# Kernel tuning notes

Measured on AMD Instinct MI355X. Metric: run time of the kernel, lower is better.

The kernel has to match this reference:

```python
import jax, jax.numpy as jnp
import numpy as np

D_MODEL = 256
N_LEVELS = 4
N_HEADS = 8
N_POINTS = 4
D_HEAD = D_MODEL // N_HEADS  # 32
BATCH = 8
SHAPES = np.array([[64, 64], [32, 32], [16, 16], [8, 8]], dtype=np.int32)
LEN_IN = int((SHAPES[:, 0] * SHAPES[:, 1]).sum())  # 5440
LEN_Q = LEN_IN
STARTS = np.concatenate([[0], np.cumsum(SHAPES[:, 0] * SHAPES[:, 1])[:-1]]).astype(np.int32)


def _offset_bias():
    # faithful _reset_parameters grid init for sampling_offsets bias
    thetas = np.arange(N_HEADS, dtype=np.float64) * (2.0 * np.pi / N_HEADS)
    grid = np.stack([np.cos(thetas), np.sin(thetas)], -1)
    grid = grid / np.abs(grid).max(-1, keepdims=True)
    grid = np.tile(grid[:, None, None, :], (1, N_LEVELS, N_POINTS, 1))
    grid = grid * (np.arange(N_POINTS) + 1)[None, None, :, None]
    return jnp.asarray(grid.reshape(-1), dtype=jnp.float32)


def setup_inputs() -> dict:
    key = jax.random.key(0)
    ks = jax.random.split(key, 8)
    s = 1.0 / np.sqrt(D_MODEL)
    return {
        "query": jax.random.normal(ks[0], (BATCH, LEN_Q, D_MODEL), jnp.float32),
        "reference_points": jax.random.uniform(ks[1], (BATCH, LEN_Q, N_LEVELS, 2), jnp.float32),
        "input_flatten": jax.random.normal(ks[2], (BATCH, LEN_IN, D_MODEL), jnp.float32),
        "input_spatial_shapes": jnp.asarray(SHAPES),
        "input_level_start_index": jnp.asarray(STARTS),
        "W_val": jax.random.normal(ks[3], (D_MODEL, D_MODEL), jnp.float32) * s,
        "b_val": jnp.zeros((D_MODEL,), jnp.float32),
        "W_off": jax.random.normal(ks[4], (D_MODEL, N_HEADS * N_LEVELS * N_POINTS * 2), jnp.float32) * 0.01,
        "b_off": _offset_bias(),
        "W_attn": jax.random.normal(ks[5], (D_MODEL, N_HEADS * N_LEVELS * N_POINTS), jnp.float32) * s,
        "b_attn": jnp.zeros((N_HEADS * N_LEVELS * N_POINTS,), jnp.float32),
        "W_out": jax.random.normal(ks[6], (D_MODEL, D_MODEL), jnp.float32) * s,
        "b_out": jnp.zeros((D_MODEL,), jnp.float32),
    }


def _ms_deform_attn_core(value, shapes_np, starts_np, sampling_locations, attention_weights):
    # value: (N, Lin, Hn, d); sampling_locations: (N, Lq, Hn, L, P, 2) in [0,1]
    # attention_weights: (N, Lq, Hn, L, P)
    n, lq = sampling_locations.shape[:2]
    value_t = jnp.transpose(value, (0, 2, 1, 3))  # (N, Hn, Lin, d)
    out = jnp.zeros((n, N_HEADS, lq, value.shape[-1]), value.dtype)
    for lvl in range(N_LEVELS):
        H, W = int(shapes_np[lvl, 0]), int(shapes_np[lvl, 1])
        st = int(starts_np[lvl])
        v = value_t[:, :, st:st + H * W]  # (N, Hn, H*W, d)
        loc = jnp.transpose(sampling_locations[:, :, :, lvl], (0, 2, 1, 3, 4))  # (N, Hn, Lq, P, 2)
        x = loc[..., 0] * W - 0.5
        y = loc[..., 1] * H - 0.5
        x0 = jnp.floor(x).astype(jnp.int32)
        y0 = jnp.floor(y).astype(jnp.int32)
        lx = x - x0
        ly = y - y0
        x1, y1 = x0 + 1, y0 + 1

        def gather(yc, xc):
            valid = (yc >= 0) & (yc < H) & (xc >= 0) & (xc < W)
            idx = jnp.clip(yc, 0, H - 1) * W + jnp.clip(xc, 0, W - 1)
            idx = idx.reshape(n, N_HEADS, -1)  # (N, Hn, Lq*P)
            g = jnp.take_along_axis(v, idx[..., None], axis=2)  # (N, Hn, Lq*P, d)
            return g * valid.reshape(n, N_HEADS, -1, 1)

        w00 = ((1 - lx) * (1 - ly)).reshape(n, N_HEADS, -1, 1)
        w01 = (lx * (1 - ly)).reshape(n, N_HEADS, -1, 1)
        w10 = ((1 - lx) * ly).reshape(n, N_HEADS, -1, 1)
        w11 = (lx * ly).reshape(n, N_HEADS, -1, 1)
        samp = (gather(y0, x0) * w00 + gather(y0, x1) * w01 +
                gather(y1, x0) * w10 + gather(y1, x1) * w11)
        samp = samp.reshape(n, N_HEADS, lq, N_POINTS, -1)
        aw = jnp.transpose(attention_weights[:, :, :, lvl], (0, 2, 1, 3))  # (N, Hn, Lq, P)
        out = out + (samp * aw[..., None]).sum(axis=3)
    return jnp.transpose(out, (0, 2, 1, 3)).reshape(n, lq, -1)


def reference(query, reference_points, input_flatten, input_spatial_shapes,
              input_level_start_index, W_val, b_val, W_off, b_off,
              W_attn, b_attn, W_out, b_out):
    shapes_np = np.asarray(input_spatial_shapes)
    starts_np = np.asarray(input_level_start_index)
    n, lq, _ = query.shape
    lin = input_flatten.shape[1]

    value = (input_flatten @ W_val + b_val).reshape(n, lin, N_HEADS, D_HEAD)
    off = (query @ W_off + b_off).reshape(n, lq, N_HEADS, N_LEVELS, N_POINTS, 2)
    attn = jax.nn.softmax((query @ W_attn + b_attn).reshape(n, lq, N_HEADS, N_LEVELS * N_POINTS), axis=-1)
    attn = attn.reshape(n, lq, N_HEADS, N_LEVELS, N_POINTS)

    # normalizer: (L, 2) as [W, H]
    normalizer = jnp.stack([input_spatial_shapes[:, 1], input_spatial_shapes[:, 0]], -1).astype(query.dtype)
    loc = reference_points[:, :, None, :, None, :] + off / normalizer[None, None, None, :, None, :]

    out = _ms_deform_attn_core(value, shapes_np, starts_np, loc, attn)
    return out @ W_out + b_out
```

## Files before the change

kernel.cpp:

```cpp
#include <hip/hip_runtime.h>

typedef unsigned short ushort;
typedef unsigned int uint;
typedef __bf16 bf16x8 __attribute__((ext_vector_type(8)));
typedef float floatx4 __attribute__((ext_vector_type(4)));
typedef ushort ushort8 __attribute__((ext_vector_type(8)));

constexpr int LQ = 5440;
constexpr int ROWS = 43520;

__device__ __forceinline__ ushort f2b(float f) {
  union { float f; uint i; } v; v.f = f;
  uint r = v.i + 0x7FFFu + ((v.i >> 16) & 1u);
  return (ushort)(r >> 16);
}
__device__ __forceinline__ float blo(uint u) {
  union { uint i; float f; } v; v.i = u << 16; return v.f;
}
__device__ __forceinline__ float bhi(uint u) {
  union { uint i; float f; } v; v.i = u & 0xFFFF0000u; return v.f;
}

__global__ __launch_bounds__(256) void wcast_kernel(
    const float* __restrict__ Wv, const float* __restrict__ Wo,
    const float* __restrict__ Wa, const float* __restrict__ Wu,
    ushort* __restrict__ Wt) {
  int k = threadIdx.x;
  int n = blockIdx.x;
  int m = blockIdx.y;
  const float* src = (m == 0) ? Wv : (m == 1) ? Wo : (m == 2) ? Wa : Wu;
  int N = (m == 2) ? 128 : 256;
  if (n >= N) return;
  size_t off = (size_t)m * 65536 - ((m == 3) ? 32768 : 0);
  Wt[off + (size_t)n * 256 + k] = f2b(src[(size_t)k * N + n]);
}

template<bool ABF16>
__device__ __forceinline__ void mfma_128x128(
    const void* __restrict__ Av, const ushort* __restrict__ Bt,
    int row_base, int n0, ushort* At, ushort* Bs, floatx4 (&acc)[4][4]) {
  const int t = threadIdx.x;
  const int r = t >> 1, half = t & 1;
  const int lane = t & 63, wv = t >> 6;
  const int quad = lane >> 4, l15 = lane & 15;
  const int m0w = (wv >> 1) * 64, n0w = (wv & 1) * 64;
#pragma unroll
  for (int i = 0; i < 4; ++i)
#pragma unroll
    for (int j = 0; j < 4; ++j) acc[i][j] = floatx4{0.f, 0.f, 0.f, 0.f};

  for (int k0 = 0; k0 < 256; k0 += 32) {
    if (ABF16) {
      const ushort* ap = (const ushort*)Av + (size_t)(row_base + r) * 256 + k0 + half * 16;
      *(ushort8*)&At[r * 32 + half * 16]     = *(const ushort8*)ap;
      *(ushort8*)&At[r * 32 + half * 16 + 8] = *(const ushort8*)(ap + 8);
    } else {
      const float* ap = (const float*)Av + (size_t)(row_base + r) * 256 + k0 + half * 16;
      float4 a0 = *(const float4*)ap,       a1 = *(const float4*)(ap + 4);
      float4 a2 = *(const float4*)(ap + 8), a3 = *(const float4*)(ap + 12);
      ushort8 u0, u1;
      u0[0] = f2b(a0.x); u0[1] = f2b(a0.y); u0[2] = f2b(a0.z); u0[3] = f2b(a0.w);
      u0[4] = f2b(a1.x); u0[5] = f2b(a1.y); u0[6] = f2b(a1.z); u0[7] = f2b(a1.w);
      u1[0] = f2b(a2.x); u1[1] = f2b(a2.y); u1[2] = f2b(a2.z); u1[3] = f2b(a2.w);
      u1[4] = f2b(a3.x); u1[5] = f2b(a3.y); u1[6] = f2b(a3.z); u1[7] = f2b(a3.w);
      *(ushort8*)&At[r * 32 + half * 16]     = u0;
      *(ushort8*)&At[r * 32 + half * 16 + 8] = u1;
    }
    {
      const ushort* bp = Bt + (size_t)(n0 + r) * 256 + k0 + half * 16;
      *(ushort8*)&Bs[r * 32 + half * 16]     = *(const ushort8*)bp;
      *(ushort8*)&Bs[r * 32 + half * 16 + 8] = *(const ushort8*)(bp + 8);
    }
    __syncthreads();
    bf16x8 af[4], bfv[4];
#pragma unroll
    for (int ti = 0; ti < 4; ++ti)
      af[ti] = *(const bf16x8*)&At[(m0w + ti * 16 + l15) * 32 + quad * 8];
#pragma unroll
    for (int tj = 0; tj < 4; ++tj)
      bfv[tj] = *(const bf16x8*)&Bs[(n0w + tj * 16 + l15) * 32 + quad * 8];
#pragma unroll
    for (int ti = 0; ti < 4; ++ti)
#pragma unroll
      for (int tj = 0; tj < 4; ++tj)
        acc[ti][tj] = __builtin_amdgcn_mfma_f32_16x16x32_bf16(af[ti], bfv[tj], acc[ti][tj], 0, 0, 0);
    __syncthreads();
  }
}

__global__ __launch_bounds__(256) void gemm_val_kernel(
    const float* __restrict__ X, const ushort* __restrict__ WtV,
    const float* __restrict__ bval, ushort* __restrict__ value) {
  __shared__ ushort At[4096];
  __shared__ ushort Bs[4096];
  floatx4 acc[4][4];
  int row_base = blockIdx.x * 128, n0 = blockIdx.y * 128;
  mfma_128x128<false>(X, WtV, row_base, n0, At, Bs, acc);
  const int t = threadIdx.x, lane = t & 63, wv = t >> 6;
  const int quad = lane >> 4, l15 = lane & 15;
  const int m0w = (wv >> 1) * 64, n0w = (wv & 1) * 64;
#pragma unroll
  for (int tj = 0; tj < 4; ++tj) {
    int gcol = n0 + n0w + tj * 16 + l15;
    float b = bval[gcol];
#pragma unroll
    for (int ti = 0; ti < 4; ++ti)
#pragma unroll
      for (int reg = 0; reg < 4; ++reg) {
        int grow = row_base + m0w + ti * 16 + quad * 4 + reg;
        value[(size_t)grow * 256 + gcol] = f2b(acc[ti][tj][reg] + b);
      }
  }
}

__global__ __launch_bounds__(256) void gemm_off_kernel(
    const float* __restrict__ Q, const ushort* __restrict__ WtO,
    const float* __restrict__ boff, const float* __restrict__ refp,
    float* __restrict__ tblf) {
  __shared__ ushort At[4096];
  __shared__ ushort Bs[4096];
  floatx4 acc[4][4];
  int row_base = blockIdx.x * 128, n0 = blockIdx.y * 128;
  mfma_128x128<false>(Q, WtO, row_base, n0, At, Bs, acc);
  const int t = threadIdx.x, lane = t & 63, wv = t >> 6;
  const int quad = lane >> 4, l15 = lane & 15;
  const int m0w = (wv >> 1) * 64, n0w = (wv & 1) * 64;
#pragma unroll
  for (int tj = 0; tj < 4; ++tj) {
    int gcol = n0 + n0w + tj * 16 + l15;
    float b = boff[gcol];
    int pair = gcol >> 1, xy = gcol & 1;
    int hh = pair >> 4, lp = pair & 15, l = lp >> 2;
    float lw = (float)(64 >> l);
#pragma unroll
    for (int ti = 0; ti < 4; ++ti)
#pragma unroll
      for (int reg = 0; reg < 4; ++reg) {
        int grow = row_base + m0w + ti * 16 + quad * 4 + reg;
        float ref = refp[(size_t)grow * 8 + l * 2 + xy];
        float o = acc[ti][tj][reg] + b;
        tblf[(((size_t)grow * 8 + hh) * 16 + lp) * 4 + xy] = ref * lw + o - 0.5f;
      }
  }
}

__global__ __launch_bounds__(256) void gemm_attn_kernel(
    const float* __restrict__ Q, const ushort* __restrict__ WtA,
    const float* __restrict__ battn, uint4* __restrict__ tbl) {
  __shared__ ushort At[4096];
  __shared__ ushort Bs[4096];
  floatx4 acc[4][4];
  int row_base = blockIdx.x * 128;
  mfma_128x128<false>(Q, WtA, row_base, 0, At, Bs, acc);
  const int t = threadIdx.x, lane = t & 63, wv = t >> 6;
  const int quad = lane >> 4, l15 = lane & 15;
  const int m0w = (wv >> 1) * 64;
  const int headbase = (wv & 1) * 4;
  const int lp = l15, l = lp >> 2;
  const int wd = 64 >> l;
  const int st = (l >= 1 ? 4096 : 0) + (l >= 2 ? 1024 : 0) + (l >= 3 ? 256 : 0);
#pragma unroll
  for (int tj = 0; tj < 4; ++tj) {
    int h = headbase + tj;
    float bia = battn[h * 16 + lp];
#pragma unroll
    for (int ti = 0; ti < 4; ++ti)
#pragma unroll
      for (int reg = 0; reg < 4; ++reg) {
        int grow = row_base + m0w + ti * 16 + quad * 4 + reg;
        float x = acc[ti][tj][reg] + bia;
        float m = x;
        m = fmaxf(m, __shfl_xor(m, 1, 64));
        m = fmaxf(m, __shfl_xor(m, 2, 64));
        m = fmaxf(m, __shfl_xor(m, 4, 64));
        m = fmaxf(m, __shfl_xor(m, 8, 64));
        float e = __expf(x - m);
        float s = e;
        s += __shfl_xor(s, 1, 64);
        s += __shfl_xor(s, 2, 64);
        s += __shfl_xor(s, 4, 64);
        s += __shfl_xor(s, 8, 64);
        float aw = e / s;
        uint4* slot = &tbl[((size_t)grow * 8 + h) * 16 + lp];
        uint4 sv = *slot;
        float xx = __uint_as_float(sv.x), yy = __uint_as_float(sv.y);
        float fx = floorf(xx), fy = floorf(yy);
        float lx = xx - fx, ly = yy - fy;
        int x0 = (int)fx, y0 = (int)fy, x1 = x0 + 1, y1 = y0 + 1;
        int cx0 = min(max(x0, 0), wd - 1), cx1 = min(max(x1, 0), wd - 1);
        int cy0 = min(max(y0, 0), wd - 1), cy1 = min(max(y1, 0), wd - 1);
        float vx0 = (x0 >= 0 && x0 < wd) ? 1.f : 0.f;
        float vx1 = (x1 >= 0 && x1 < wd) ? 1.f : 0.f;
        float vy0 = (y0 >= 0 && y0 < wd) ? 1.f : 0.f;
        float vy1 = (y1 >= 0 && y1 < wd) ? 1.f : 0.f;
        float g00 = (1.f - lx) * (1.f - ly) * vx0 * vy0 * aw;
        float g01 = lx * (1.f - ly) * vx1 * vy0 * aw;
        float g10 = (1.f - lx) * ly * vx0 * vy1 * aw;
        float g11 = lx * ly * vx1 * vy1 * aw;
        uint i00 = st + cy0 * wd + cx0, i01 = st + cy0 * wd + cx1;
        uint i10 = st + cy1 * wd + cx0, i11 = st + cy1 * wd + cx1;
        uint4 ov;
        ov.x = i00 | (i01 << 16);
        ov.y = i10 | (i11 << 16);
        ov.z = (uint)f2b(g00) | ((uint)f2b(g01) << 16);
        ov.w = (uint)f2b(g10) | ((uint)f2b(g11) << 16);
        *slot = ov;
      }
  }
}

__global__ __launch_bounds__(512) void core_kernel(
    const ushort* __restrict__ value, const uint* __restrict__ tbl,
    uint* __restrict__ coreo) {
  const int brow = blockIdx.x;
  const int b = brow / LQ;
  const int t = threadIdx.x;
  const int h = t >> 6, lane = t & 63;
  const int d2 = lane & 15;
  const uint v = tbl[((size_t)brow * 8 + h) * 64 + lane];
  const uint* vb = (const uint*)(value + (size_t)b * (LQ * 256)) + h * 16 + d2;
  float acc0 = 0.f, acc1 = 0.f;
#pragma unroll
  for (int j = 0; j < 4; ++j) {
    uint i01 = (uint)__shfl((int)v, (lane & 48) | (4 * j + 0), 64);
    uint i23 = (uint)__shfl((int)v, (lane & 48) | (4 * j + 1), 64);
    uint wab = (uint)__shfl((int)v, (lane & 48) | (4 * j + 2), 64);
    uint wcd = (uint)__shfl((int)v, (lane & 48) | (4 * j + 3), 64);
    uint s00 = vb[(i01 & 0xFFFFu) * 128];
    uint s01 = vb[(i01 >> 16) * 128];
    uint s10 = vb[(i23 & 0xFFFFu) * 128];
    uint s11 = vb[(i23 >> 16) * 128];
    float f00 = blo(wab), f01 = bhi(wab), f10 = blo(wcd), f11 = bhi(wcd);
    acc0 = fmaf(f00, blo(s00), acc0); acc1 = fmaf(f00, bhi(s00), acc1);
    acc0 = fmaf(f01, blo(s01), acc0); acc1 = fmaf(f01, bhi(s01), acc1);
    acc0 = fmaf(f10, blo(s10), acc0); acc1 = fmaf(f10, bhi(s10), acc1);
    acc0 = fmaf(f11, blo(s11), acc0); acc1 = fmaf(f11, bhi(s11), acc1);
  }
  acc0 += __shfl_xor(acc0, 16, 64); acc0 += __shfl_xor(acc0, 32, 64);
  acc1 += __shfl_xor(acc1, 16, 64); acc1 += __shfl_xor(acc1, 32, 64);
  if (lane < 16) {
    uint p = (uint)f2b(acc0) | ((uint)f2b(acc1) << 16);
    coreo[((size_t)brow * 8 + h) * 16 + d2] = p;
  }
}

__global__ __launch_bounds__(256) void gemm_out_kernel(
    const ushort* __restrict__ C, const ushort* __restrict__ WtU,
    const float* __restrict__ bout, float* __restrict__ out) {
  __shared__ ushort At[4096];
  __shared__ ushort Bs[4096];
  floatx4 acc[4][4];
  int row_base = blockIdx.x * 128, n0 = blockIdx.y * 128;
  mfma_128x128<true>(C, WtU, row_base, n0, At, Bs, acc);
  const int t = threadIdx.x, lane = t & 63, wv = t >> 6;
  const int quad = lane >> 4, l15 = lane & 15;
  const int m0w = (wv >> 1) * 64, n0w = (wv & 1) * 64;
#pragma unroll
  for (int tj = 0; tj < 4; ++tj) {
    int gcol = n0 + n0w + tj * 16 + l15;
    float b = bout[gcol];
#pragma unroll
    for (int ti = 0; ti < 4; ++ti)
#pragma unroll
      for (int reg = 0; reg < 4; ++reg) {
        int grow = row_base + m0w + ti * 16 + quad * 4 + reg;
        out[(size_t)grow * 256 + gcol] = acc[ti][tj][reg] + b;
      }
  }
}

extern "C" void kernel_launch(void* const* d_in, const int* in_sizes, int n_in,
                              void* d_out, int out_size, void* d_ws, size_t ws_size,
                              hipStream_t stream) {
  const float* query  = (const float*)d_in[0];
  const float* refp   = (const float*)d_in[1];
  const float* inpf   = (const float*)d_in[2];
  const float* W_val  = (const float*)d_in[5];
  const float* b_val  = (const float*)d_in[6];
  const float* W_off  = (const float*)d_in[7];
  const float* b_off  = (const float*)d_in[8];
  const float* W_attn = (const float*)d_in[9];
  const float* b_attn = (const float*)d_in[10];
  const float* W_out  = (const float*)d_in[11];
  const float* b_out  = (const float*)d_in[12];

  char* ws = (char*)d_ws;
  ushort* Wt    = (ushort*)ws;
  ushort* value = (ushort*)(ws + 1048576);
  uint*   tbl   = (uint*)(ws + 1048576 + 22282240);
  uint*   coreo = (uint*)(ws + 1048576 + 22282240 + 89128960);

  dim3 blk(256);
  wcast_kernel    <<<dim3(256, 4), blk, 0, stream>>>(W_val, W_off, W_attn, W_out, Wt);
  gemm_val_kernel <<<dim3(ROWS / 128, 2), blk, 0, stream>>>(inpf, Wt, b_val, value);
  gemm_off_kernel <<<dim3(ROWS / 128, 2), blk, 0, stream>>>(query, Wt + 65536, b_off, refp, (float*)tbl);
  gemm_attn_kernel<<<dim3(ROWS / 128, 1), blk, 0, stream>>>(query, Wt + 131072, b_attn, (uint4*)tbl);
  core_kernel     <<<dim3(ROWS), dim3(512), 0, stream>>>(value, tbl, coreo);
  gemm_out_kernel <<<dim3(ROWS / 128, 2), blk, 0, stream>>>((const ushort*)coreo, Wt + 163840, b_out, (float*)d_out);
}
```

Measured before the change: 387.8 us.

## Precast activations to bf16, retile attn GEMM, widen core gathers, batch-interleave rows

Adds a precast kernel that converts query and input_flatten to bf16 once, so the GEMMs stop re-converting fp32 tiles inside their K loops (query had been converted twice, by the off and attn GEMMs). The attention GEMM now uses 64-row tiles and stages its logits through shared memory so each thread does a full 16-way softmax without shuffles. The value and offset epilogues pack pairs of outputs into wider stores. The core gather kernel reads 8-byte uint2 chunks, interleaves blocks across batches, and reuses workspace regions. The precast adds an extra pass over the fp32 inputs, and the workspace aliasing depends on kernel ordering being correct.

New measurement: 443.1 us. 1.14x slower.

```diff
diff --git a/kernel.cpp b/kernel.cpp
--- a/kernel.cpp
+++ b/kernel.cpp
@@ -19,6 +19,21 @@
 }
 __device__ __forceinline__ float bhi(uint u) {
   union { uint i; float f; } v; v.i = u & 0xFFFF0000u; return v.f;
+}
+
+__global__ __launch_bounds__(256) void precast_kernel(
+    const float* __restrict__ q, const float* __restrict__ x,
+    ushort* __restrict__ qb, ushort* __restrict__ ib) {
+  int bx = blockIdx.x;
+  const float* src; ushort* dst;
+  if (bx < 5440) { src = q; dst = qb; } else { src = x; dst = ib; bx -= 5440; }
+  size_t i = ((size_t)bx * 256 + threadIdx.x) * 8;
+  float4 a = *(const float4*)(src + i);
+  float4 b = *(const float4*)(src + i + 4);
+  ushort8 o;
+  o[0] = f2b(a.x); o[1] = f2b(a.y); o[2] = f2b(a.z); o[3] = f2b(a.w);
+  o[4] = f2b(b.x); o[5] = f2b(b.y); o[6] = f2b(b.z); o[7] = f2b(b.w);
+  *(ushort8*)(dst + i) = o;
 }
 
 __global__ __launch_bounds__(256) void wcast_kernel(
@@ -35,9 +50,8 @@
   Wt[off + (size_t)n * 256 + k] = f2b(src[(size_t)k * N + n]);
 }
 
-template<bool ABF16>
-__device__ __forceinline__ void mfma_128x128(
-    const void* __restrict__ Av, const ushort* __restrict__ Bt,
+__device__ __forceinline__ void mfma_tile128(
+    const ushort* __restrict__ Ab, const ushort* __restrict__ Bt,
     int row_base, int n0, ushort* At, ushort* Bs, floatx4 (&acc)[4][4]) {
   const int t = threadIdx.x;
   const int r = t >> 1, half = t & 1;
@@ -50,21 +64,10 @@
     for (int j = 0; j < 4; ++j) acc[i][j] = floatx4{0.f, 0.f, 0.f, 0.f};
 
   for (int k0 = 0; k0 < 256; k0 += 32) {
-    if (ABF16) {
-      const ushort* ap = (const ushort*)Av + (size_t)(row_base + r) * 256 + k0 + half * 16;
+    {
+      const ushort* ap = Ab + (size_t)(row_base + r) * 256 + k0 + half * 16;
       *(ushort8*)&At[r * 32 + half * 16]     = *(const ushort8*)ap;
       *(ushort8*)&At[r * 32 + half * 16 + 8] = *(const ushort8*)(ap + 8);
-    } else {
-      const float* ap = (const float*)Av + (size_t)(row_base + r) * 256 + k0 + half * 16;
-      float4 a0 = *(const float4*)ap,       a1 = *(const float4*)(ap + 4);
-      float4 a2 = *(const float4*)(ap + 8), a3 = *(const float4*)(ap + 12);
-      ushort8 u0, u1;
-      u0[0] = f2b(a0.x); u0[1] = f2b(a0.y); u0[2] = f2b(a0.z); u0[3] = f2b(a0.w);
-      u0[4] = f2b(a1.x); u0[5] = f2b(a1.y); u0[6] = f2b(a1.z); u0[7] = f2b(a1.w);
-      u1[0] = f2b(a2.x); u1[1] = f2b(a2.y); u1[2] = f2b(a2.z); u1[3] = f2b(a2.w);
-      u1[4] = f2b(a3.x); u1[5] = f2b(a3.y); u1[6] = f2b(a3.z); u1[7] = f2b(a3.w);
-      *(ushort8*)&At[r * 32 + half * 16]     = u0;
-      *(ushort8*)&At[r * 32 + half * 16 + 8] = u1;
     }
     {
       const ushort* bp = Bt + (size_t)(n0 + r) * 256 + k0 + half * 16;
@@ -89,13 +92,13 @@
 }
 
 __global__ __launch_bounds__(256) void gemm_val_kernel(
-    const float* __restrict__ X, const ushort* __restrict__ WtV,
-    const float* __restrict__ bval, ushort* __restrict__ value) {
+    const ushort* __restrict__ Xb, const ushort* __restrict__ WtV,
+    const float* __restrict__ bval, uint* __restrict__ value32) {
   __shared__ ushort At[4096];
   __shared__ ushort Bs[4096];
   floatx4 acc[4][4];
   int row_base = blockIdx.x * 128, n0 = blockIdx.y * 128;
-  mfma_128x128<false>(X, WtV, row_base, n0, At, Bs, acc);
+  mfma_tile128(Xb, WtV, row_base, n0, At, Bs, acc);
   const int t = threadIdx.x, lane = t & 63, wv = t >> 6;
   const int quad = lane >> 4, l15 = lane & 15;
   const int m0w = (wv >> 1) * 64, n0w = (wv & 1) * 64;
@@ -108,20 +111,25 @@
 #pragma unroll
       for (int reg = 0; reg < 4; ++reg) {
         int grow = row_base + m0w + ti * 16 + quad * 4 + reg;
-        value[(size_t)grow * 256 + gcol] = f2b(acc[ti][tj][reg] + b);
+        float val = acc[ti][tj][reg] + b;
+        float part = __shfl_xor(val, 1, 64);
+        if ((l15 & 1) == 0) {
+          uint p = (uint)f2b(val) | ((uint)f2b(part) << 16);
+          value32[(size_t)grow * 128 + (gcol >> 1)] = p;
+        }
       }
   }
 }
 
 __global__ __launch_bounds__(256) void gemm_off_kernel(
-    const float* __restrict__ Q, const ushort* __restrict__ WtO,
+    const ushort* __restrict__ Qb, const ushort* __restrict__ WtO,
     const float* __restrict__ boff, const float* __restrict__ refp,
     float* __restrict__ tblf) {
   __shared__ ushort At[4096];
   __shared__ ushort Bs[4096];
   floatx4 acc[4][4];
   int row_base = blockIdx.x * 128, n0 = blockIdx.y * 128;
-  mfma_128x128<false>(Q, WtO, row_base, n0, At, Bs, acc);
+  mfma_tile128(Qb, WtO, row_base, n0, At, Bs, acc);
   const int t = threadIdx.x, lane = t & 63, wv = t >> 6;
   const int quad = lane >> 4, l15 = lane & 15;
   const int m0w = (wv >> 1) * 64, n0w = (wv & 1) * 64;
@@ -138,109 +146,162 @@
       for (int reg = 0; reg < 4; ++reg) {
         int grow = row_base + m0w + ti * 16 + quad * 4 + reg;
         float ref = refp[(size_t)grow * 8 + l * 2 + xy];
-        float o = acc[ti][tj][reg] + b;
-        tblf[(((size_t)grow * 8 + hh) * 16 + lp) * 4 + xy] = ref * lw + o - 0.5f;
+        float pos = ref * lw + (acc[ti][tj][reg] + b) - 0.5f;
+        float part = __shfl_xor(pos, 1, 64);
+        if ((l15 & 1) == 0) {
+          float2 o; o.x = pos; o.y = part;
+          *(float2*)(tblf + (((size_t)grow * 8 + hh) * 16 + lp) * 4) = o;
+        }
       }
   }
 }
 
+union KU {
+  struct { ushort At[2048]; ushort Bs[4096]; } g;
+  float ct[64 * 132];
+  __device__ KU() {}
+};
 __global__ __launch_bounds__(256) void gemm_attn_kernel(
-    const float* __restrict__ Q, const ushort* __restrict__ WtA,
-    const float* __restrict__ battn, uint4* __restrict__ tbl) {
-  __shared__ ushort At[4096];
-  __shared__ ushort Bs[4096];
-  floatx4 acc[4][4];
-  int row_base = blockIdx.x * 128;
-  mfma_128x128<false>(Q, WtA, row_base, 0, At, Bs, acc);
-  const int t = threadIdx.x, lane = t & 63, wv = t >> 6;
-  const int quad = lane >> 4, l15 = lane & 15;
-  const int m0w = (wv >> 1) * 64;
-  const int headbase = (wv & 1) * 4;
-  const int lp = l15, l = lp >> 2;
-  const int wd = 64 >> l;
-  const int st = (l >= 1 ? 4096 : 0) + (l >= 2 ? 1024 : 0) + (l >= 3 ? 256 : 0);
-#pragma unroll
-  for (int tj = 0; tj < 4; ++tj) {
-    int h = headbase + tj;
-    float bia = battn[h * 16 + lp];
-#pragma unroll
-    for (int ti = 0; ti < 4; ++ti)
-#pragma unroll
-      for (int reg = 0; reg < 4; ++reg) {
-        int grow = row_base + m0w + ti * 16 + quad * 4 + reg;
-        float x = acc[ti][tj][reg] + bia;
-        float m = x;
-        m = fmaxf(m, __shfl_xor(m, 1, 64));
-        m = fmaxf(m, __shfl_xor(m, 2, 64));
-        m = fmaxf(m, __shfl_xor(m, 4, 64));
-        m = fmaxf(m, __shfl_xor(m, 8, 64));
-        float e = __expf(x - m);
-        float s = e;
-        s += __shfl_xor(s, 1, 64);
-        s += __shfl_xor(s, 2, 64);
-        s += __shfl_xor(s, 4, 64);
-        s += __shfl_xor(s, 8, 64);
-        float aw = e / s;
-        uint4* slot = &tbl[((size_t)grow * 8 + h) * 16 + lp];
-        uint4 sv = *slot;
-        float xx = __uint_as_float(sv.x), yy = __uint_as_float(sv.y);
-        float fx = floorf(xx), fy = floorf(yy);
-        float lx = xx - fx, ly = yy - fy;
-        int x0 = (int)fx, y0 = (int)fy, x1 = x0 + 1, y1 = y0 + 1;
-        int cx0 = min(max(x0, 0), wd - 1), cx1 = min(max(x1, 0), wd - 1);
-        int cy0 = min(max(y0, 0), wd - 1), cy1 = min(max(y1, 0), wd - 1);
-        float vx0 = (x0 >= 0 && x0 < wd) ? 1.f : 0.f;
-        float vx1 = (x1 >= 0 && x1 < wd) ? 1.f : 0.f;
-        float vy0 = (y0 >= 0 && y0 < wd) ? 1.f : 0.f;
-        float vy1 = (y1 >= 0 && y1 < wd) ? 1.f : 0.f;
-        float g00 = (1.f - lx) * (1.f - ly) * vx0 * vy0 * aw;
-        float g01 = lx * (1.f - ly) * vx1 * vy0 * aw;
-        float g10 = (1.f - lx) * ly * vx0 * vy1 * aw;
-        float g11 = lx * ly * vx1 * vy1 * aw;
-        uint i00 = st + cy0 * wd + cx0, i01 = st + cy0 * wd + cx1;
-        uint i10 = st + cy1 * wd + cx0, i11 = st + cy1 * wd + cx1;
-        uint4 ov;
-        ov.x = i00 | (i01 << 16);
-        ov.y = i10 | (i11 << 16);
-        ov.z = (uint)f2b(g00) | ((uint)f2b(g01) << 16);
-        ov.w = (uint)f2b(g10) | ((uint)f2b(g11) << 16);
-        *slot = ov;
-      }
+    const ushort* __restrict__ Qb, const ushort* __restrict__ WtA,
+    const float* __restrict__ battn, uint4* __restrict__ tblq) {
+  __shared__ KU u;
+  floatx4 acc[8];
+  const int t = threadIdx.x;
+  const int lane = t & 63, wv = t >> 6;
+  const int quad = lane >> 4, l15 = lane & 15;
+  int row_base = blockIdx.x * 64;
+#pragma unroll
+  for (int j = 0; j < 8; ++j) acc[j] = floatx4{0.f, 0.f, 0.f, 0.f};
+
+  for (int k0 = 0; k0 < 256; k0 += 32) {
+    {
+      int r = t >> 2, seg = t & 3;
+      *(ushort8*)&u.g.At[r * 32 + seg * 8] =
+          *(const ushort8*)(Qb + (size_t)(row_base + r) * 256 + k0 + seg * 8);
+    }
+#pragma unroll
+    for (int i = 0; i < 2; ++i) {
+      int item = t + 256 * i;
+      int r = item >> 2, seg = item & 3;
+      *(ushort8*)&u.g.Bs[r * 32 + seg * 8] =
+          *(const ushort8*)(WtA + (size_t)r * 256 + k0 + seg * 8);
+    }
+    __syncthreads();
+    bf16x8 af = *(const bf16x8*)&u.g.At[(wv * 16 + l15) * 32 + quad * 8];
+#pragma unroll
+    for (int tj = 0; tj < 8; ++tj) {
+      bf16x8 bf = *(const bf16x8*)&u.g.Bs[(tj * 16 + l15) * 32 + quad * 8];
+      acc[tj] = __builtin_amdgcn_mfma_f32_16x16x32_bf16(af, bf, acc[tj], 0, 0, 0);
+    }
+    __syncthreads();
+  }
+#pragma unroll
+  for (int tj = 0; tj < 8; ++tj) {
+    int col = tj * 16 + l15;
+    float bb = battn[col];
+#pragma unroll
+    for (int reg = 0; reg < 4; ++reg) {
+      int rr = wv * 16 + quad * 4 + reg;
+      u.ct[rr * 132 + col] = acc[tj][reg] + bb;
+    }
+  }
+  __syncthreads();
+#pragma unroll
+  for (int i = 0; i < 2; ++i) {
+    int gidx = t + 256 * i;
+    int row = gidx >> 3, h = gidx & 7;
+    int grow = row_base + row;
+    float xv[16];
+    *(float4*)&xv[0]  = *(const float4*)&u.ct[row * 132 + h * 16];
+    *(float4*)&xv[4]  = *(const float4*)&u.ct[row * 132 + h * 16 + 4];
+    *(float4*)&xv[8]  = *(const float4*)&u.ct[row * 132 + h * 16 + 8];
+    *(float4*)&xv[12] = *(const float4*)&u.ct[row * 132 + h * 16 + 12];
+    float m = xv[0];
+#pragma unroll
+    for (int j = 1; j < 16; ++j) m = fmaxf(m, xv[j]);
+    float ssum = 0.f;
+#pragma unroll
+    for (int j = 0; j < 16; ++j) { xv[j] = __expf(xv[j] - m); ssum += xv[j]; }
+    float inv = 1.f / ssum;
+    size_t sbase = ((size_t)grow * 8 + h) * 16;
+#pragma unroll
+    for (int j = 0; j < 16; ++j) {
+      const int l = j >> 2;
+      const int wd = 64 >> l;
+      const int st = (l == 0) ? 0 : (l == 1) ? 4096 : (l == 2) ? 5120 : 5376;
+      uint4* sp = &tblq[sbase + j];
+      float2 xy = *(const float2*)sp;
+      float aw = xv[j] * inv;
+      float fx = floorf(xy.x), fy = floorf(xy.y);
+      float lx = xy.x - fx, ly = xy.y - fy;
+      int x0 = (int)fx, y0 = (int)fy, x1 = x0 + 1, y1 = y0 + 1;
+      int cx0 = min(max(x0, 0), wd - 1), cx1 = min(max(x1, 0), wd - 1);
+      int cy0 = min(max(y0, 0), wd - 1), cy1 = min(max(y1, 0), wd - 1);
+      float vx0 = (x0 >= 0 && x0 < wd) ? 1.f : 0.f;
+      float vx1 = (x1 >= 0 && x1 < wd) ? 1.f : 0.f;
+      float vy0 = (y0 >= 0 && y0 < wd) ? 1.f : 0.f;
+      float vy1 = (y1 >= 0 && y1 < wd) ? 1.f : 0.f;
+      float g00 = (1.f - lx) * (1.f - ly) * vx0 * vy0 * aw;
+      float g01 = lx * (1.f - ly) * vx1 * vy0 * aw;
+      float g10 = (1.f - lx) * ly * vx0 * vy1 * aw;
+      float g11 = lx * ly * vx1 * vy1 * aw;
+      uint i00 = st + cy0 * wd + cx0, i01 = st + cy0 * wd + cx1;
+      uint i10 = st + cy1 * wd + cx0, i11 = st + cy1 * wd + cx1;
+      uint4 ov;
+      ov.x = i00 | (i01 << 16);
+      ov.y = i10 | (i11 << 16);
+      ov.z = (uint)f2b(g00) | ((uint)f2b(g01) << 16);
+      ov.w = (uint)f2b(g10) | ((uint)f2b(g11) << 16);
+      *sp = ov;
+    }
   }
 }
 
 __global__ __launch_bounds__(512) void core_kernel(
-    const ushort* __restrict__ value, const uint* __restrict__ tbl,
-    uint* __restrict__ coreo) {
-  const int brow = blockIdx.x;
-  const int b = brow / LQ;
+    const uint* __restrict__ value32, const uint* __restrict__ tbl32,
+    uint* __restrict__ coreo32) {
+  const int bx = blockIdx.x;
+  const int b = bx & 7;
+  const int brow = b * LQ + (bx >> 3);
   const int t = threadIdx.x;
   const int h = t >> 6, lane = t & 63;
-  const int d2 = lane & 15;
-  const uint v = tbl[((size_t)brow * 8 + h) * 64 + lane];
-  const uint* vb = (const uint*)(value + (size_t)b * (LQ * 256)) + h * 16 + d2;
-  float acc0 = 0.f, acc1 = 0.f;
-#pragma unroll
-  for (int j = 0; j < 4; ++j) {
-    uint i01 = (uint)__shfl((int)v, (lane & 48) | (4 * j + 0), 64);
-    uint i23 = (uint)__shfl((int)v, (lane & 48) | (4 * j + 1), 64);
-    uint wab = (uint)__shfl((int)v, (lane & 48) | (4 * j + 2), 64);
-    uint wcd = (uint)__shfl((int)v, (lane & 48) | (4 * j + 3), 64);
-    uint s00 = vb[(i01 & 0xFFFFu) * 128];
-    uint s01 = vb[(i01 >> 16) * 128];
-    uint s10 = vb[(i23 & 0xFFFFu) * 128];
-    uint s11 = vb[(i23 >> 16) * 128];
-    float f00 = blo(wab), f01 = bhi(wab), f10 = blo(wcd), f11 = bhi(wcd);
-    acc0 = fmaf(f00, blo(s00), acc0); acc1 = fmaf(f00, bhi(s00), acc1);
-    acc0 = fmaf(f01, blo(s01), acc0); acc1 = fmaf(f01, bhi(s01), acc1);
-    acc0 = fmaf(f10, blo(s10), acc0); acc1 = fmaf(f10, bhi(s10), acc1);
-    acc0 = fmaf(f11, blo(s11), acc0); acc1 = fmaf(f11, bhi(s11), acc1);
-  }
-  acc0 += __shfl_xor(acc0, 16, 64); acc0 += __shfl_xor(acc0, 32, 64);
-  acc1 += __shfl_xor(acc1, 16, 64); acc1 += __shfl_xor(acc1, 32, 64);
-  if (lane < 16) {
-    uint p = (uint)f2b(acc0) | ((uint)f2b(acc1) << 16);
-    coreo[((size_t)brow * 8 + h) * 16 + d2] = p;
+  const int s = lane >> 3, g = lane & 7;
+  const uint v = tbl32[((size_t)brow * 8 + h) * 64 + lane];
+  const uint2* vb = (const uint2*)value32 + (size_t)b * (LQ * 64) + h * 8 + g;
+  float a0 = 0.f, a1 = 0.f, a2 = 0.f, a3 = 0.f;
+#pragma unroll
+  for (int lpi = 0; lpi < 2; ++lpi) {
+    int base4 = (s + lpi * 8) * 4;
+    uint i01 = (uint)__shfl((int)v, base4 + 0, 64);
+    uint i23 = (uint)__shfl((int)v, base4 + 1, 64);
+    uint wab = (uint)__shfl((int)v, base4 + 2, 64);
+    uint wcd = (uint)__shfl((int)v, base4 + 3, 64);
+    uint2 v00 = vb[(size_t)(i01 & 0xFFFFu) * 64];
+    uint2 v01 = vb[(size_t)(i01 >> 16) * 64];
+    uint2 v10 = vb[(size_t)(i23 & 0xFFFFu) * 64];
+    uint2 v11 = vb[(size_t)(i23 >> 16) * 64];
+    float w00 = blo(wab), w01 = bhi(wab), w10 = blo(wcd), w11 = bhi(wcd);
+    a0 = fmaf(w00, blo(v00.x), a0); a1 = fmaf(w00, bhi(v00.x), a1);
+    a2 = fmaf(w00, blo(v00.y), a2); a3 = fmaf(w00, bhi(v00.y), a3);
+    a0 = fmaf(w01, blo(v01.x), a0); a1 = fmaf(w01, bhi(v01.x), a1);
+    a2 = fmaf(w01, blo(v01.y), a2); a3 = fmaf(w01, bhi(v01.y), a3);
+    a0 = fmaf(w10, blo(v10.x), a0); a1 = fmaf(w10, bhi(v10.x), a1);
+    a2 = fmaf(w10, blo(v10.y), a2); a3 = fmaf(w10, bhi(v10.y), a3);
+    a0 = fmaf(w11, blo(v11.x), a0); a1 = fmaf(w11, bhi(v11.x), a1);
+    a2 = fmaf(w11, blo(v11.y), a2); a3 = fmaf(w11, bhi(v11.y), a3);
+  }
+#pragma unroll
+  for (int m = 8; m <= 32; m <<= 1) {
+    a0 += __shfl_xor(a0, m, 64);
+    a1 += __shfl_xor(a1, m, 64);
+    a2 += __shfl_xor(a2, m, 64);
+    a3 += __shfl_xor(a3, m, 64);
+  }
+  if (s == 0) {
+    uint2 o;
+    o.x = (uint)f2b(a0) | ((uint)f2b(a1) << 16);
+    o.y = (uint)f2b(a2) | ((uint)f2b(a3) << 16);
+    *(uint2*)(coreo32 + (size_t)brow * 128 + h * 16 + g * 2) = o;
   }
 }
 
@@ -251,7 +312,7 @@
   __shared__ ushort Bs[4096];
   floatx4 acc[4][4];
   int row_base = blockIdx.x * 128, n0 = blockIdx.y * 128;
-  mfma_128x128<true>(C, WtU, row_base, n0, At, Bs, acc);
+  mfma_tile128(C, WtU, row_base, n0, At, Bs, acc);
   const int t = threadIdx.x, lane = t & 63, wv = t >> 6;
   const int quad = lane >> 4, l15 = lane & 15;
   const int m0w = (wv >> 1) * 64, n0w = (wv & 1) * 64;
@@ -286,15 +347,18 @@
 
   char* ws = (char*)d_ws;
   ushort* Wt    = (ushort*)ws;
-  ushort* value = (ushort*)(ws + 1048576);
-  uint*   tbl   = (uint*)(ws + 1048576 + 22282240);
-  uint*   coreo = (uint*)(ws + 1048576 + 22282240 + 89128960);
+  ushort* qb    = (ushort*)(ws + 1048576);
+  uint*   value = (uint*)(ws + 23330816);
+  uint*   tbl   = (uint*)(ws + 45613056);
+  ushort* ib    = (ushort*)(ws + 45613056);
+  uint*   coreo = (uint*)(ws + 1048576);
 
   dim3 blk(256);
+  precast_kernel  <<<dim3(10880), blk, 0, stream>>>(query, inpf, qb, ib);
   wcast_kernel    <<<dim3(256, 4), blk, 0, stream>>>(W_val, W_off, W_attn, W_out, Wt);
-  gemm_val_kernel <<<dim3(ROWS / 128, 2), blk, 0, stream>>>(inpf, Wt, b_val, value);
-  gemm_off_kernel <<<dim3(ROWS / 128, 2), blk, 0, stream>>>(query, Wt + 65536, b_off, refp, (float*)tbl);
-  gemm_attn_kernel<<<dim3(ROWS / 128, 1), blk, 0, stream>>>(query, Wt + 131072, b_attn, (uint4*)tbl);
+  gemm_val_kernel <<<dim3(340, 2), blk, 0, stream>>>(ib, Wt, b_val, value);
+  gemm_off_kernel <<<dim3(340, 2), blk, 0, stream>>>(qb, Wt + 65536, b_off, refp, (float*)tbl);
+  gemm_attn_kernel<<<dim3(680), blk, 0, stream>>>(qb, Wt + 131072, b_attn, (uint4*)tbl);
   core_kernel     <<<dim3(ROWS), dim3(512), 0, stream>>>(value, tbl, coreo);
-  gemm_out_kernel <<<dim3(ROWS / 128, 2), blk, 0, stream>>>((const ushort*)coreo, Wt + 163840, b_out, (float*)d_out);
-}
+  gemm_out_kernel <<<dim3(340, 2), blk, 0, stream>>>((const ushort*)coreo, Wt + 163840, b_out, (float*)d_out);
+}
```
